# Kernel optimization log

Measured on AMD Instinct MI355X. Metric: run time of the kernel, lower is better.

## Reference

```python
import jax, jax.numpy as jnp
import numpy as np


def setup_inputs() -> dict:
    key = jax.random.key(0)
    k1, k2, k3 = jax.random.split(key, 3)
    G, E, C, H, I = 1, 8, 2048, 1024, 4096
    x = jax.random.normal(k1, (G, E, C, H), dtype=jnp.float32)
    # init per module.reset_parameters: normal std sqrt(0.1/hidden) and sqrt(0.1/intermediate)
    wi = jax.random.normal(k2, (E, H, I), dtype=jnp.float32) * np.sqrt(0.1 / H)
    wo = jax.random.normal(k3, (E, I, H), dtype=jnp.float32) * np.sqrt(0.1 / I)
    return {"x": x, "wi": wi, "wo": wo}


def reference(x, wi, wo):
    # x: [G, E, C, H] -> transpose to [E, G, C, H] -> [E, G*C, H]
    G, E, C, H = x.shape
    xt = jnp.swapaxes(x, 0, 1).reshape(E, G * C, H)
    # per-expert grouped GEMM: hidden -> intermediate, gelu, -> hidden
    h = jax.nn.gelu(jnp.einsum("eth,ehi->eti", xt, wi), approximate=False)
    out = jnp.einsum("eti,eih->eth", h, wo)
    out = out.reshape(E, G, C, H)
    return jnp.swapaxes(out, 0, 1)  # [G, E, C, H]
```

## Files before the change

kernel.cpp:

```cpp
#include <hip/hip_runtime.h>
#include <hip/hip_bf16.h>
#include <cstdint>

typedef __attribute__((ext_vector_type(4))) float f32x4;
typedef __attribute__((ext_vector_type(8))) short bf16x8;
typedef __attribute__((ext_vector_type(4))) short s16x4;
typedef __attribute__((ext_vector_type(8))) short s16x8;

__device__ __forceinline__ short f2bf(float f) {
    union { float f; unsigned u; } v; v.f = f;
    unsigned r = v.u + 0x7FFFu + ((v.u >> 16) & 1u);
    return (short)(r >> 16);
}

__global__ __launch_bounds__(256) void cast_bf16(const float* __restrict__ in,
                                                 short* __restrict__ out, long n) {
    long i = ((long)blockIdx.x * 256 + threadIdx.x) * 8;
    if (i + 7 < n) {
        float4 a = *(const float4*)(in + i);
        float4 b = *(const float4*)(in + i + 4);
        s16x8 o;
        o[0] = f2bf(a.x); o[1] = f2bf(a.y); o[2] = f2bf(a.z); o[3] = f2bf(a.w);
        o[4] = f2bf(b.x); o[5] = f2bf(b.y); o[6] = f2bf(b.z); o[7] = f2bf(b.w);
        *(s16x8*)(out + i) = o;
    }
}

__global__ __launch_bounds__(256) void transpose_cast(const float* __restrict__ in,
                                                      short* __restrict__ out,
                                                      int R, int C) {
    __shared__ float t[64][65];
    const size_t eoff = (size_t)blockIdx.z * R * C;
    in  += eoff;
    out += eoff;
    const int c0 = blockIdx.x * 64, r0 = blockIdx.y * 64;
    const int tid = threadIdx.x;
    const int rr  = tid >> 4;
    const int cc4 = (tid & 15) * 4;
    #pragma unroll
    for (int i = 0; i < 4; ++i) {
        const int row = i * 16 + rr;
        float4 v = *(const float4*)(in + (size_t)(r0 + row) * C + c0 + cc4);
        t[row][cc4 + 0] = v.x; t[row][cc4 + 1] = v.y;
        t[row][cc4 + 2] = v.z; t[row][cc4 + 3] = v.w;
    }
    __syncthreads();
    #pragma unroll
    for (int i = 0; i < 4; ++i) {
        const int oc = i * 16 + rr;
        s16x4 o;
        o[0] = f2bf(t[cc4 + 0][oc]);
        o[1] = f2bf(t[cc4 + 1][oc]);
        o[2] = f2bf(t[cc4 + 2][oc]);
        o[3] = f2bf(t[cc4 + 3][oc]);
        *(s16x4*)(out + (size_t)(c0 + oc) * R + r0 + cc4) = o;
    }
}


#define FENCE() asm volatile("" ::: "memory")
#define BARRIER() do { FENCE(); __builtin_amdgcn_s_barrier(); FENCE(); } while (0)

__device__ __forceinline__ void stage_half(const short* __restrict__ g,
                                           short* l, const size_t* goff) {
    __builtin_amdgcn_global_load_lds(
        (const __attribute__((address_space(1))) void*)(g + goff[0]),
        (__attribute__((address_space(3))) void*)l, 16, 0, 0);
    __builtin_amdgcn_global_load_lds(
        (const __attribute__((address_space(1))) void*)(g + goff[1]),
        (__attribute__((address_space(3))) void*)(l + 4096), 16, 0, 0);
}

template <int FUSE>
__global__ __launch_bounds__(512, 2) void gemm_bt(const short* __restrict__ A,
                                                  const short* __restrict__ Bt,
                                                  void* __restrict__ Cout,
                                                  int M, int N, int K) {
    __shared__ short lds[65536];
    const int tid  = threadIdx.x;
    const int lane = tid & 63;
    const int wave = tid >> 6;
    const int wm   = wave >> 2;
    const int wn   = wave & 3;

    const int tilesM = M >> 8;
    const int perE   = tilesM * (N >> 8);
    const int total  = gridDim.x * gridDim.z;
    int lin = blockIdx.z * gridDim.x + blockIdx.x;
    lin = (lin & 7) * (total >> 3) + (lin >> 3);
    const int e   = lin / perE;
    const int rem = lin - e * perE;
    const int m0  = (rem % tilesM) << 8;
    const int n0  = (rem / tilesM) << 8;

    const short* Ab = A  + (size_t)e * M * K + (size_t)m0 * K;
    const short* Bb = Bt + (size_t)e * N * K + (size_t)n0 * K;
    const size_t hK = (size_t)128 * K;

    size_t goff[2];
    #pragma unroll
    for (int i = 0; i < 2; ++i) {
        const int p  = i * 512 + tid;
        const int r  = p >> 3;
        const int sp = p & 7;
        goff[i] = (size_t)r * K + (size_t)((sp ^ (r & 7)) << 3);
    }
    const int lwb = wave * 512;

    const int lrow = lane & 15, lq = lane >> 4;
    int offA[8], offB[4];
    #pragma unroll
    for (int m = 0; m < 8; ++m) {
        const int rh = m * 16 + lrow;
        offA[m] = wm * 8192 + rh * 64 + ((lq ^ (rh & 7)) << 3);
    }
    #pragma unroll
    for (int n = 0; n < 4; ++n) {
        const int row = wn * 64 + n * 16 + lrow;
        const int h = row >> 7, rh = row & 127;
        offB[n] = 16384 + h * 8192 + rh * 64 + ((lq ^ (rh & 7)) << 3);
    }

    f32x4 acc[8][4] = {};
    const int nk = K >> 6;

    stage_half(Ab,      lds +     0 + lwb, goff);
    stage_half(Ab + hK, lds +  8192 + lwb, goff);
    stage_half(Bb,      lds + 16384 + lwb, goff);
    stage_half(Bb + hK, lds + 24576 + lwb, goff);
    if (nk > 1) {
        const short* A1p = Ab + 64;
        const short* B1p = Bb + 64;
        stage_half(B1p,      lds + 32768 + 16384 + lwb, goff);
        stage_half(B1p + hK, lds + 32768 + 24576 + lwb, goff);
        stage_half(A1p,      lds + 32768 +     0 + lwb, goff);
        asm volatile("s_waitcnt vmcnt(6)" ::: "memory");
    } else {
        asm volatile("s_waitcnt vmcnt(0)" ::: "memory");
    }
    BARRIER();

    bf16x8 Af[4][2], Bf0[2][2], Bf1[2][2];

    for (int t = 0; t < nk; ++t) {
        const int sl  = (t & 1) << 15;
        const int slN = ((t + 1) & 1) << 15;
        const short* S = lds + sl;
        const short* An1 = Ab + (size_t)(t + 1) * 64;
        const short* An2 = Ab + (size_t)(t + 2) * 64;
        const short* Bn2 = Bb + (size_t)(t + 2) * 64;

        #pragma unroll
        for (int i = 0; i < 4; ++i) {
            const int o = offA[i];
            Af[i][0] = *(const bf16x8*)(S + o);
            Af[i][1] = *(const bf16x8*)(S + (o ^ 32));
        }
        #pragma unroll
        for (int j = 0; j < 2; ++j) {
            const int o = offB[j];
            Bf0[j][0] = *(const bf16x8*)(S + o);
            Bf0[j][1] = *(const bf16x8*)(S + (o ^ 32));
        }
        if (t + 1 < nk) stage_half(An1 + hK, lds + slN + 8192 + lwb, goff);
        BARRIER();
        __builtin_amdgcn_s_setprio(1);
        #pragma unroll
        for (int s = 0; s < 2; ++s)
            #pragma unroll
            for (int i = 0; i < 4; ++i)
                #pragma unroll
                for (int j = 0; j < 2; ++j)
                    acc[i][j] = __builtin_amdgcn_mfma_f32_16x16x32_bf16(
                        Af[i][s], Bf0[j][s], acc[i][j], 0, 0, 0);
        __builtin_amdgcn_s_setprio(0);
        BARRIER();

        #pragma unroll
        for (int j = 0; j < 2; ++j) {
            const int o = offB[2 + j];
            Bf1[j][0] = *(const bf16x8*)(S + o);
            Bf1[j][1] = *(const bf16x8*)(S + (o ^ 32));
        }
        BARRIER();
        __builtin_amdgcn_s_setprio(1);
        #pragma unroll
        for (int s = 0; s < 2; ++s)
            #pragma unroll
            for (int i = 0; i < 4; ++i)
                #pragma unroll
                for (int j = 0; j < 2; ++j)
                    acc[i][2 + j] = __builtin_amdgcn_mfma_f32_16x16x32_bf16(
                        Af[i][s], Bf1[j][s], acc[i][2 + j], 0, 0, 0);
        __builtin_amdgcn_s_setprio(0);
        BARRIER();

        #pragma unroll
        for (int i = 0; i < 4; ++i) {
            const int o = offA[4 + i];
            Af[i][0] = *(const bf16x8*)(S + o);
            Af[i][1] = *(const bf16x8*)(S + (o ^ 32));
        }
        if (t + 2 < nk) stage_half(Bn2, lds + sl + 16384 + lwb, goff);
        BARRIER();
        __builtin_amdgcn_s_setprio(1);
        #pragma unroll
        for (int s = 0; s < 2; ++s)
            #pragma unroll
            for (int i = 0; i < 4; ++i)
                #pragma unroll
                for (int j = 0; j < 2; ++j)
                    acc[4 + i][2 + j] = __builtin_amdgcn_mfma_f32_16x16x32_bf16(
                        Af[i][s], Bf1[j][s], acc[4 + i][2 + j], 0, 0, 0);
        __builtin_amdgcn_s_setprio(0);
        BARRIER();

        if (t + 2 < nk) {
            stage_half(Bn2 + hK, lds + sl + 24576 + lwb, goff);
            stage_half(An2,      lds + sl +     0 + lwb, goff);
            asm volatile("s_waitcnt vmcnt(6)" ::: "memory");
        } else {
            asm volatile("s_waitcnt vmcnt(0)" ::: "memory");
        }
        BARRIER();
        __builtin_amdgcn_s_setprio(1);
        #pragma unroll
        for (int s = 0; s < 2; ++s)
            #pragma unroll
            for (int i = 0; i < 4; ++i)
                #pragma unroll
                for (int j = 0; j < 2; ++j)
                    acc[4 + i][j] = __builtin_amdgcn_mfma_f32_16x16x32_bf16(
                        Af[i][s], Bf0[j][s], acc[4 + i][j], 0, 0, 0);
        __builtin_amdgcn_s_setprio(0);
        BARRIER();
    }

    const int r0q = lq << 2;
    const int cL  = lane & 15;
    if (FUSE) {
        short* C = (short*)Cout + (size_t)e * M * N;
        #pragma unroll
        for (int m = 0; m < 8; ++m)
            #pragma unroll
            for (int n = 0; n < 4; ++n)
                #pragma unroll
                for (int rr = 0; rr < 4; ++rr) {
                    const int row = m0 + wm * 128 + m * 16 + r0q + rr;
                    const int col = n0 + wn * 64 + n * 16 + cL;
                    float v = acc[m][n][rr];
                    v = 0.5f * v * (1.0f + erff(v * 0.70710678118654752f));
                    C[(size_t)row * N + col] = f2bf(v);
                }
    } else {
        float* C = (float*)Cout + (size_t)e * M * N;
        #pragma unroll
        for (int m = 0; m < 8; ++m)
            #pragma unroll
            for (int n = 0; n < 4; ++n)
                #pragma unroll
                for (int rr = 0; rr < 4; ++rr) {
                    const int row = m0 + wm * 128 + m * 16 + r0q + rr;
                    const int col = n0 + wn * 64 + n * 16 + cL;
                    C[(size_t)row * N + col] = acc[m][n][rr];
                }
    }
}

extern "C" void kernel_launch(void* const* d_in, const int* in_sizes, int n_in,
                              void* d_out, int out_size, void* d_ws, size_t ws_size,
                              hipStream_t stream) {
    constexpr int E = 8, Ct = 2048, H = 1024, I = 4096;

    const float* x  = (const float*)d_in[0];
    const float* wi = (const float*)d_in[1];
    const float* wo = (const float*)d_in[2];
    float* out = (float*)d_out;

    char* ws = (char*)d_ws;
    short* xb  = (short*)(ws);
    short* wiT = (short*)(ws + (size_t)33554432);
    short* woT = (short*)(ws + (size_t)100663296);
    short* h   = (short*)(ws + (size_t)167772160);

    {
        long n = (long)E * Ct * H;
        cast_bf16<<<dim3((unsigned)(n / 2048)), dim3(256), 0, stream>>>(x, xb, n);
    }
    transpose_cast<<<dim3(I / 64, H / 64, E), dim3(256), 0, stream>>>(wi, wiT, H, I);
    transpose_cast<<<dim3(H / 64, I / 64, E), dim3(256), 0, stream>>>(wo, woT, I, H);

    gemm_bt<1><<<dim3(128, 1, E), dim3(512), 0, stream>>>(xb, wiT, (void*)h, Ct, I, H);

    gemm_bt<0><<<dim3(32, 1, E), dim3(512), 0, stream>>>(h, woT, (void*)out, Ct, H, I);
}
```

Baseline: 614.3 us.

## Merge MFMA phases into two clusters and batch global staging loads

Restructures the main loop of the grouped GEMM so the four small MFMA phases, each fenced by barriers, become two larger clusters. Each cluster covers a full 64-row A half against all four B fragments. All four next-stage global-to-LDS staging loads are now issued together after the first barrier, cutting the barriers per K-step from eight to two. This removes workgroup synchronisation stalls and gives the scheduler longer uninterrupted MFMA runs. The trade-off is that prefetch loads for the next tile start later in the iteration, leaving less compute to hide global memory latency.

```diff
diff --git a/kernel.cpp b/kernel.cpp
--- a/kernel.cpp
+++ b/kernel.cpp
@@ -162,38 +162,28 @@
             Bf0[j][0] = *(const bf16x8*)(S + o);
             Bf0[j][1] = *(const bf16x8*)(S + (o ^ 32));
         }
-        if (t + 1 < nk) stage_half(An1 + hK, lds + slN + 8192 + lwb, goff);
-        BARRIER();
-        __builtin_amdgcn_s_setprio(1);
-        #pragma unroll
-        for (int s = 0; s < 2; ++s)
-            #pragma unroll
-            for (int i = 0; i < 4; ++i)
-                #pragma unroll
-                for (int j = 0; j < 2; ++j)
-                    acc[i][j] = __builtin_amdgcn_mfma_f32_16x16x32_bf16(
-                        Af[i][s], Bf0[j][s], acc[i][j], 0, 0, 0);
-        __builtin_amdgcn_s_setprio(0);
-        BARRIER();
-
         #pragma unroll
         for (int j = 0; j < 2; ++j) {
             const int o = offB[2 + j];
             Bf1[j][0] = *(const bf16x8*)(S + o);
             Bf1[j][1] = *(const bf16x8*)(S + (o ^ 32));
         }
-        BARRIER();
+
         __builtin_amdgcn_s_setprio(1);
         #pragma unroll
         for (int s = 0; s < 2; ++s)
             #pragma unroll
-            for (int i = 0; i < 4; ++i)
+            for (int i = 0; i < 4; ++i) {
+                #pragma unroll
+                for (int j = 0; j < 2; ++j)
+                    acc[i][j] = __builtin_amdgcn_mfma_f32_16x16x32_bf16(
+                        Af[i][s], Bf0[j][s], acc[i][j], 0, 0, 0);
                 #pragma unroll
                 for (int j = 0; j < 2; ++j)
                     acc[i][2 + j] = __builtin_amdgcn_mfma_f32_16x16x32_bf16(
                         Af[i][s], Bf1[j][s], acc[i][2 + j], 0, 0, 0);
+            }
         __builtin_amdgcn_s_setprio(0);
-        BARRIER();
 
         #pragma unroll
         for (int i = 0; i < 4; ++i) {
@@ -201,38 +191,34 @@
             Af[i][0] = *(const bf16x8*)(S + o);
             Af[i][1] = *(const bf16x8*)(S + (o ^ 32));
         }
-        if (t + 2 < nk) stage_half(Bn2, lds + sl + 16384 + lwb, goff);
+
         BARRIER();
+
+        if (t + 1 < nk) stage_half(An1 + hK, lds + slN + 8192 + lwb, goff);
+        if (t + 2 < nk) {
+            stage_half(Bn2,      lds + sl + 16384 + lwb, goff);
+            stage_half(Bn2 + hK, lds + sl + 24576 + lwb, goff);
+            stage_half(An2,      lds + sl +     0 + lwb, goff);
+        }
+
         __builtin_amdgcn_s_setprio(1);
         #pragma unroll
         for (int s = 0; s < 2; ++s)
             #pragma unroll
-            for (int i = 0; i < 4; ++i)
+            for (int i = 0; i < 4; ++i) {
+                #pragma unroll
+                for (int j = 0; j < 2; ++j)
+                    acc[4 + i][j] = __builtin_amdgcn_mfma_f32_16x16x32_bf16(
+                        Af[i][s], Bf0[j][s], acc[4 + i][j], 0, 0, 0);
                 #pragma unroll
                 for (int j = 0; j < 2; ++j)
                     acc[4 + i][2 + j] = __builtin_amdgcn_mfma_f32_16x16x32_bf16(
                         Af[i][s], Bf1[j][s], acc[4 + i][2 + j], 0, 0, 0);
+            }
         __builtin_amdgcn_s_setprio(0);
-        BARRIER();
-
-        if (t + 2 < nk) {
-            stage_half(Bn2 + hK, lds + sl + 24576 + lwb, goff);
-            stage_half(An2,      lds + sl +     0 + lwb, goff);
-            asm volatile("s_waitcnt vmcnt(6)" ::: "memory");
-        } else {
-            asm volatile("s_waitcnt vmcnt(0)" ::: "memory");
-        }
-        BARRIER();
-        __builtin_amdgcn_s_setprio(1);
-        #pragma unroll
-        for (int s = 0; s < 2; ++s)
-            #pragma unroll
-            for (int i = 0; i < 4; ++i)
-                #pragma unroll
-                for (int j = 0; j < 2; ++j)
-                    acc[4 + i][j] = __builtin_amdgcn_mfma_f32_16x16x32_bf16(
-                        Af[i][s], Bf0[j][s], acc[4 + i][j], 0, 0, 0);
-        __builtin_amdgcn_s_setprio(0);
+
+        if (t + 2 < nk) asm volatile("s_waitcnt vmcnt(6)" ::: "memory");
+        else            asm volatile("s_waitcnt vmcnt(0)" ::: "memory");
         BARRIER();
     }
 
```

New measurement: 628.8 us. +2.4%, slower.
